# Kernel tuning notes

Measured on AMD Instinct MI355X. Metric: run time of the kernel, lower is better.

The kernel has to match this reference:

```python
import jax, jax.numpy as jnp
import numpy as np

N_NODES = 50000


def setup_inputs() -> dict:
    key = jax.random.key(0)
    k1, k2, k3, k4 = jax.random.split(key, 4)
    x = jax.random.normal(k1, (N_NODES, 128), dtype=jnp.float32)
    edge_index = jax.random.randint(k2, (2, 800000), 0, N_NODES, dtype=jnp.int64)
    W = jax.random.normal(k3, (128, 128), dtype=jnp.float32) * 0.05
    b = jax.random.normal(k4, (128,), dtype=jnp.float32) * 0.05
    return {"x": x, "edge_index": edge_index, "W": W, "b": b}


def reference(x, edge_index, W, b):
    # x: [N, C_in], edge_index: [2, E]
    row, col = edge_index[0], edge_index[1]
    n = x.shape[0]
    # degree of each node as a source (bincount over row)
    deg = jax.ops.segment_sum(jnp.ones_like(row, dtype=x.dtype), row, num_segments=n)
    # deg^{-1/2} with inf -> 0 (deg == 0 case)
    deg_inv_sqrt = jnp.where(deg > 0, jax.lax.rsqrt(jnp.maximum(deg, 1.0)) * jnp.where(deg > 0, 1.0, 0.0), 0.0)
    deg_inv_sqrt = jnp.where(deg > 0, deg ** -0.5, 0.0)
    norm = deg_inv_sqrt[row] * deg_inv_sqrt[col]  # [E]
    # gather, scale, scatter-add: agg[row] += x[col] * norm
    msgs = x[col] * norm[:, None]  # [E, C_in]
    agg = jax.ops.segment_sum(msgs, row, num_segments=n)  # [N, C_in]
    # linear
    return agg @ W.T + b
```

## Files before the change

kernel.cpp:

```cpp
#include <hip/hip_runtime.h>
#include <hip/hip_bf16.h>


typedef short v8s __attribute__((ext_vector_type(8)));
typedef float v4f __attribute__((ext_vector_type(4)));

#define ELLCAP 64
#define NSHARD 32
#define SUBCAP 224
#define ROWSTRIDE 136

static __device__ __forceinline__ unsigned int f2bf(float f) {
    __hip_bfloat16 h = __float2bfloat16(f);
    return (unsigned int)__builtin_bit_cast(unsigned short, h);
}

__global__ __launch_bounds__(256) void k_bin(
    const int* __restrict__ idx, int* __restrict__ gbin,
    unsigned int* __restrict__ pairs, const float4* __restrict__ w4,
    ushort4* __restrict__ wb4, const float2* __restrict__ x2,
    unsigned int* __restrict__ xs32, int E, int ncast, int N, int nbins) {
    int b = blockIdx.x;
    const int t = threadIdx.x;
    if (b < 16) {
        int i = b * 256 + t;
        float4 v = w4[i];
        ushort4 o;
        o.x = (unsigned short)f2bf(v.x);
        o.y = (unsigned short)f2bf(v.y);
        o.z = (unsigned short)f2bf(v.z);
        o.w = (unsigned short)f2bf(v.w);
        wb4[i] = o;
        return;
    }
    b -= 16;
    if (b < ncast) {
        int base = b * 4096;
#pragma unroll 4
        for (int it = 0; it < 16; ++it) {
            int i = base + it * 256 + t;
            int lr = i >> 6;
            unsigned ov = 0u;
            if (lr < N) {
                float2 v = x2[i];
                ov = f2bf(v.x) | (f2bf(v.y) << 16);
            }
            xs32[i] = ov;
        }
        return;
    }
    b -= ncast;
    __shared__ int hist[256];
    __shared__ int hist2[256];
    __shared__ int base[256];
    hist[t] = 0;
    hist2[t] = 0;
    __syncthreads();

    int e0 = b * 2048 + t * 8;
    int nv = E - e0;
    nv = nv > 8 ? 8 : (nv < 0 ? 0 : nv);
    int rows[8], cols[8];
    if (nv == 8) {
        int4 a0 = *(const int4*)&idx[e0];
        int4 a1 = *(const int4*)&idx[e0 + 4];
        int4 c0 = *(const int4*)&idx[E + e0];
        int4 c1 = *(const int4*)&idx[E + e0 + 4];
        rows[0] = a0.x; rows[1] = a0.y; rows[2] = a0.z; rows[3] = a0.w;
        rows[4] = a1.x; rows[5] = a1.y; rows[6] = a1.z; rows[7] = a1.w;
        cols[0] = c0.x; cols[1] = c0.y; cols[2] = c0.z; cols[3] = c0.w;
        cols[4] = c1.x; cols[5] = c1.y; cols[6] = c1.z; cols[7] = c1.w;
    } else {
        for (int k = 0; k < 8; ++k) {
            rows[k] = (k < nv) ? idx[e0 + k] : 0;
            cols[k] = (k < nv) ? idx[E + e0 + k] : 0;
        }
    }
#pragma unroll
    for (int k = 0; k < 8; ++k)
        if (k < nv) atomicAdd(&hist[rows[k] >> 8], 1);
    __syncthreads();
    const int shard = b & (NSHARD - 1);
    if (t < nbins)
        base[t] = atomicAdd(&gbin[t * NSHARD + shard], hist[t]);
    int loc[8];
#pragma unroll
    for (int k = 0; k < 8; ++k)
        loc[k] = (k < nv) ? atomicAdd(&hist2[rows[k] >> 8], 1) : 0;
    __syncthreads();
#pragma unroll
    for (int k = 0; k < 8; ++k) {
        if (k < nv) {
            int bin = rows[k] >> 8;
            int pos = base[bin] + loc[k];
            if (pos < SUBCAP)
                pairs[((size_t)bin * NSHARD + shard) * SUBCAP + pos] =
                    (unsigned)(((rows[k] & 255) << 16) | cols[k]);
        }
    }
}

__global__ __launch_bounds__(1024) void k_deg(
    const unsigned int* __restrict__ pairs, const int* __restrict__ gbin,
    float* __restrict__ dis, int N) {
    __shared__ int cnt[256];
    __shared__ int scnt[NSHARD];
    const int bin = blockIdx.x;
    const int t = threadIdx.x;
    if (t < 256) cnt[t] = 0;
    if (t < NSHARD) {
        int m = gbin[bin * NSHARD + t];
        scnt[t] = m > SUBCAP ? SUBCAP : m;
    }
    __syncthreads();
    for (int s = 0; s < NSHARD; ++s) {
        int ms = scnt[s];
        size_t pb = ((size_t)bin * NSHARD + s) * SUBCAP;
        for (int i = t; i < ms; i += 1024)
            atomicAdd(&cnt[pairs[pb + i] >> 16], 1);
    }
    __syncthreads();
    if (t < 256) {
        int r = bin * 256 + t;
        int d = cnt[t];
        dis[r] = (r < N && d > 0) ? rsqrtf((float)d) : 0.f;
    }
}

__global__ __launch_bounds__(256) void k_fused(
    const unsigned int* __restrict__ pairs, const int* __restrict__ gbin,
    const float* __restrict__ dis, const unsigned int* __restrict__ xs32,
    const v8s* __restrict__ Wb8, const float* __restrict__ bias,
    float* __restrict__ out, int N) {
    __shared__ __align__(16) unsigned short lell[32 * ELLCAP];
    __shared__ int cnt[32];
    __shared__ int scnt[NSHARD];
    __shared__ __align__(16) unsigned short smem[32 * ROWSTRIDE];
    const int bin = blockIdx.x >> 3, sub = blockIdx.x & 7;
    const int t = threadIdx.x;
    if (t < 32) cnt[t] = 0;
    else if (t >= 64 && t < 64 + NSHARD) {
        int m = gbin[bin * NSHARD + (t - 64)];
        scnt[t - 64] = m > SUBCAP ? SUBCAP : m;
    }
    __syncthreads();
    for (int s = 0; s < NSHARD; ++s) {
        int ms = scnt[s];
        size_t pb = ((size_t)bin * NSHARD + s) * SUBCAP;
        for (int i = t; i < ms; i += 256) {
            unsigned pv = pairs[pb + i];
            int lr = pv >> 16;
            if ((lr >> 5) == sub) {
                int la = lr & 31;
                int slot = atomicAdd(&cnt[la], 1);
                if (slot < ELLCAP)
                    lell[la * ELLCAP + slot] = (unsigned short)(pv & 0xFFFF);
            }
        }
    }
    __syncthreads();

    const int wv = t >> 6, lane = t & 63;
    const int r0 = bin * 256 + sub * 32;
    for (int i = 0; i < 8; ++i) {
        int lrow = wv * 8 + i;
        int n = r0 + lrow;
        float acc0 = 0.f, acc1 = 0.f;
        if (n < N) {
            int dtrue = cnt[lrow];
            int d = dtrue > ELLCAP ? ELLCAP : dtrue;
            int cl = lell[lrow * ELLCAP + lane];
            int c = (lane < d) ? cl : N;
            float dcf = dis[c];
            int dcb = __builtin_bit_cast(int, dcf);
            for (int j = 0; j < d; j += 16) {
                int cc[16];
#pragma unroll
                for (int u = 0; u < 16; ++u)
                    cc[u] = __builtin_amdgcn_readlane(c, j + u);
                unsigned uu[16];
#pragma unroll
                for (int u = 0; u < 16; ++u)
                    uu[u] = xs32[(size_t)cc[u] * 64 + lane];
                float sc[16];
#pragma unroll
                for (int u = 0; u < 16; ++u)
                    sc[u] = __builtin_bit_cast(
                        float, __builtin_amdgcn_readlane(dcb, j + u));
#pragma unroll
                for (int u = 0; u < 16; ++u) {
                    acc0 = fmaf(sc[u], __builtin_bit_cast(float, uu[u] << 16), acc0);
                    acc1 = fmaf(sc[u],
                                __builtin_bit_cast(float, uu[u] & 0xFFFF0000u), acc1);
                }
            }
            float s = (dtrue > 0) ? rsqrtf((float)dtrue) : 0.f;
            acc0 *= s;
            acc1 *= s;
        }
        unsigned pack = f2bf(acc0) | (f2bf(acc1) << 16);
        *(unsigned int*)&smem[(size_t)lrow * ROWSTRIDE + lane * 2] = pack;
    }
    __syncthreads();

    {
        int quad = lane >> 4, m16 = lane & 15;
        int lrow = (wv & 1) * 16 + m16;
        v8s afrag[4];
#pragma unroll
        for (int kk = 0; kk < 4; ++kk)
            afrag[kk] = *(const v8s*)&smem[lrow * ROWSTRIDE + kk * 32 + quad * 8];
        int rbase = r0 + (wv & 1) * 16 + quad * 4;
        int jbase = (wv >> 1) * 64;
#pragma unroll
        for (int jt = 0; jt < 4; ++jt) {
            int jcol = jbase + jt * 16 + m16;
            v4f acc = {0.f, 0.f, 0.f, 0.f};
#pragma unroll
            for (int kk = 0; kk < 4; ++kk) {
                v8s bfrag = Wb8[jcol * 16 + kk * 4 + quad];
                acc = __builtin_amdgcn_mfma_f32_16x16x32_bf16(afrag[kk], bfrag,
                                                              acc, 0, 0, 0);
            }
            float bj = bias[jcol];
#pragma unroll
            for (int r = 0; r < 4; ++r) {
                int row = rbase + r;
                if (row < N) out[(size_t)row * 128 + jcol] = acc[r] + bj;
            }
        }
    }
}

extern "C" void kernel_launch(void* const* d_in, const int* in_sizes, int n_in,
                              void* d_out, int out_size, void* d_ws, size_t ws_size,
                              hipStream_t stream) {
    const float* x = (const float*)d_in[0];
    const int* idx = (const int*)d_in[1];
    const float* W = (const float*)d_in[2];
    const float* b = (const float*)d_in[3];
    float* out = (float*)d_out;

    const int N = in_sizes[0] / 128;
    const int E = in_sizes[1] / 2;
    const int nbins = (N + 255) / 256;
    const int nrows = nbins * 256;
    const int ncast = nbins * 4;

    char* p = (char*)d_ws;
    auto alloc = [&](size_t bytes) {
        char* r = p;
        p += (bytes + 63) & ~(size_t)63;
        return r;
    };
    int* gbin = (int*)alloc((size_t)nbins * NSHARD * 4);
    unsigned int* pairs =
        (unsigned int*)alloc((size_t)nbins * NSHARD * SUBCAP * 4);
    float* dis = (float*)alloc((size_t)nrows * 4);
    unsigned int* xs = (unsigned int*)alloc((size_t)nrows * 128 * 2);
    ushort4* wb = (ushort4*)alloc(128 * 128 * 2);

    hipMemsetAsync(gbin, 0, (size_t)nbins * NSHARD * sizeof(int), stream);

    const int bblocks = 16 + ncast + (E + 2047) / 2048;
    k_bin<<<bblocks, 256, 0, stream>>>(idx, gbin, pairs, (const float4*)W, wb,
                                       (const float2*)x, xs, E, ncast, N, nbins);
    k_deg<<<nbins, 1024, 0, stream>>>(pairs, gbin, dis, N);
    k_fused<<<nbins * 8, 256, 0, stream>>>(pairs, gbin, dis, xs, (const v8s*)wb,
                                           b, out, N);
}
```

Measured before the change: 158.7 us.

## Build ELL adjacency once in degree kernel instead of per fused block

The degree kernel now builds the full per-bin ELL neighbor list in shared memory and writes it, together with clamped degree counts, to global memory. Previously each of the 8 fused blocks per bin rescanned all 32 shards of pairs and kept only its own rows. The fused kernel now just loads its ELL rows and degrees directly and prefetches all 8 rows' neighbor indices and scales before the gather loop. This adds a global ELL write/read (about 6.4 MB) and a 32 KB shared-memory buffer in the degree kernel in exchange for removing the redundant 8x rescan of the pairs buffer.

```diff
diff --git a/kernel.cpp b/kernel.cpp
--- a/kernel.cpp
+++ b/kernel.cpp
@@ -100,106 +100,106 @@
     }
 }
 
-__global__ __launch_bounds__(1024) void k_deg(
+__global__ __launch_bounds__(1024) void k_ell(
     const unsigned int* __restrict__ pairs, const int* __restrict__ gbin,
+    unsigned short* __restrict__ ell, unsigned char* __restrict__ degc,
     float* __restrict__ dis, int N) {
+    __shared__ __align__(16) unsigned short lell[256 * ELLCAP];
     __shared__ int cnt[256];
-    __shared__ int scnt[NSHARD];
     const int bin = blockIdx.x;
     const int t = threadIdx.x;
     if (t < 256) cnt[t] = 0;
-    if (t < NSHARD) {
-        int m = gbin[bin * NSHARD + t];
-        scnt[t] = m > SUBCAP ? SUBCAP : m;
-    }
-    __syncthreads();
-    for (int s = 0; s < NSHARD; ++s) {
-        int ms = scnt[s];
-        size_t pb = ((size_t)bin * NSHARD + s) * SUBCAP;
-        for (int i = t; i < ms; i += 1024)
-            atomicAdd(&cnt[pairs[pb + i] >> 16], 1);
-    }
-    __syncthreads();
+    __syncthreads();
+
+    {
+        const int g = t >> 5, l32 = t & 31;
+        int m = gbin[bin * NSHARD + g];
+        m = m > SUBCAP ? SUBCAP : m;
+        size_t pb = ((size_t)bin * NSHARD + g) * SUBCAP;
+        for (int i = l32; i < m; i += 32) {
+            unsigned pv = pairs[pb + i];
+            int la = pv >> 16;
+            int slot = atomicAdd(&cnt[la], 1);
+            if (slot < ELLCAP)
+                lell[la * ELLCAP + slot] = (unsigned short)(pv & 0xFFFF);
+        }
+    }
+    __syncthreads();
+
     if (t < 256) {
         int r = bin * 256 + t;
         int d = cnt[t];
-        dis[r] = (r < N && d > 0) ? rsqrtf((float)d) : 0.f;
+        if (r < N) {
+            dis[r] = (d > 0) ? rsqrtf((float)d) : 0.f;
+            degc[r] = (unsigned char)(d > ELLCAP ? ELLCAP : d);
+        } else {
+            dis[r] = 0.f;
+        }
+    }
+
+    {
+        unsigned int* gell = (unsigned int*)(ell + (size_t)bin * 256 * ELLCAP);
+        const unsigned int* sell = (const unsigned int*)lell;
+        for (int i = t; i < 8192; i += 1024) gell[i] = sell[i];
     }
 }
 
 __global__ __launch_bounds__(256) void k_fused(
-    const unsigned int* __restrict__ pairs, const int* __restrict__ gbin,
+    const unsigned short* __restrict__ ell, const unsigned char* __restrict__ degc,
     const float* __restrict__ dis, const unsigned int* __restrict__ xs32,
     const v8s* __restrict__ Wb8, const float* __restrict__ bias,
     float* __restrict__ out, int N) {
-    __shared__ __align__(16) unsigned short lell[32 * ELLCAP];
-    __shared__ int cnt[32];
-    __shared__ int scnt[NSHARD];
     __shared__ __align__(16) unsigned short smem[32 * ROWSTRIDE];
-    const int bin = blockIdx.x >> 3, sub = blockIdx.x & 7;
-    const int t = threadIdx.x;
-    if (t < 32) cnt[t] = 0;
-    else if (t >= 64 && t < 64 + NSHARD) {
-        int m = gbin[bin * NSHARD + (t - 64)];
-        scnt[t - 64] = m > SUBCAP ? SUBCAP : m;
-    }
-    __syncthreads();
-    for (int s = 0; s < NSHARD; ++s) {
-        int ms = scnt[s];
-        size_t pb = ((size_t)bin * NSHARD + s) * SUBCAP;
-        for (int i = t; i < ms; i += 256) {
-            unsigned pv = pairs[pb + i];
-            int lr = pv >> 16;
-            if ((lr >> 5) == sub) {
-                int la = lr & 31;
-                int slot = atomicAdd(&cnt[la], 1);
-                if (slot < ELLCAP)
-                    lell[la * ELLCAP + slot] = (unsigned short)(pv & 0xFFFF);
-            }
-        }
-    }
-    __syncthreads();
-
-    const int wv = t >> 6, lane = t & 63;
-    const int r0 = bin * 256 + sub * 32;
+    const int nb0 = blockIdx.x * 32;
+    const int wv = threadIdx.x >> 6, lane = threadIdx.x & 63;
+    const int rowbase = nb0 + wv * 8;
+
+    int d8[8], c8[8];
+    float dv8[8];
+#pragma unroll
     for (int i = 0; i < 8; ++i) {
-        int lrow = wv * 8 + i;
-        int n = r0 + lrow;
+        int n = rowbase + i;
+        int d = (n < N) ? degc[n] : 0;
+        d8[i] = __builtin_amdgcn_readfirstlane(d);
+        int cl = (n < N) ? ell[(size_t)n * ELLCAP + lane] : 0;
+        c8[i] = (lane < d8[i]) ? cl : N;
+    }
+#pragma unroll
+    for (int i = 0; i < 8; ++i) dv8[i] = dis[c8[i]];
+
+#pragma unroll
+    for (int i = 0; i < 8; ++i) {
+        int n = rowbase + i;
         float acc0 = 0.f, acc1 = 0.f;
-        if (n < N) {
-            int dtrue = cnt[lrow];
-            int d = dtrue > ELLCAP ? ELLCAP : dtrue;
-            int cl = lell[lrow * ELLCAP + lane];
-            int c = (lane < d) ? cl : N;
-            float dcf = dis[c];
-            int dcb = __builtin_bit_cast(int, dcf);
-            for (int j = 0; j < d; j += 16) {
-                int cc[16];
-#pragma unroll
-                for (int u = 0; u < 16; ++u)
-                    cc[u] = __builtin_amdgcn_readlane(c, j + u);
-                unsigned uu[16];
-#pragma unroll
-                for (int u = 0; u < 16; ++u)
-                    uu[u] = xs32[(size_t)cc[u] * 64 + lane];
-                float sc[16];
-#pragma unroll
-                for (int u = 0; u < 16; ++u)
-                    sc[u] = __builtin_bit_cast(
-                        float, __builtin_amdgcn_readlane(dcb, j + u));
-#pragma unroll
-                for (int u = 0; u < 16; ++u) {
-                    acc0 = fmaf(sc[u], __builtin_bit_cast(float, uu[u] << 16), acc0);
-                    acc1 = fmaf(sc[u],
-                                __builtin_bit_cast(float, uu[u] & 0xFFFF0000u), acc1);
-                }
-            }
-            float s = (dtrue > 0) ? rsqrtf((float)dtrue) : 0.f;
-            acc0 *= s;
-            acc1 *= s;
-        }
+        int d = d8[i];
+        int c = c8[i];
+        int dcb = __builtin_bit_cast(int, dv8[i]);
+        for (int j = 0; j < d; j += 16) {
+            int cc[16];
+#pragma unroll
+            for (int u = 0; u < 16; ++u)
+                cc[u] = __builtin_amdgcn_readlane(c, j + u);
+            unsigned uu[16];
+#pragma unroll
+            for (int u = 0; u < 16; ++u)
+                uu[u] = xs32[(size_t)cc[u] * 64 + lane];
+            float sc[16];
+#pragma unroll
+            for (int u = 0; u < 16; ++u)
+                sc[u] = __builtin_bit_cast(float,
+                                           __builtin_amdgcn_readlane(dcb, j + u));
+#pragma unroll
+            for (int u = 0; u < 16; ++u) {
+                acc0 = fmaf(sc[u], __builtin_bit_cast(float, uu[u] << 16), acc0);
+                acc1 = fmaf(sc[u],
+                            __builtin_bit_cast(float, uu[u] & 0xFFFF0000u), acc1);
+            }
+        }
+        float s = dis[n];
+        acc0 *= s;
+        acc1 *= s;
         unsigned pack = f2bf(acc0) | (f2bf(acc1) << 16);
-        *(unsigned int*)&smem[(size_t)lrow * ROWSTRIDE + lane * 2] = pack;
+        *(unsigned int*)&smem[(size_t)(wv * 8 + i) * ROWSTRIDE + lane * 2] = pack;
     }
     __syncthreads();
 
@@ -210,7 +210,7 @@
 #pragma unroll
         for (int kk = 0; kk < 4; ++kk)
             afrag[kk] = *(const v8s*)&smem[lrow * ROWSTRIDE + kk * 32 + quad * 8];
-        int rbase = r0 + (wv & 1) * 16 + quad * 4;
+        int rbase = nb0 + (wv & 1) * 16 + quad * 4;
         int jbase = (wv >> 1) * 64;
 #pragma unroll
         for (int jt = 0; jt < 4; ++jt) {
@@ -257,6 +257,9 @@
     unsigned int* pairs =
         (unsigned int*)alloc((size_t)nbins * NSHARD * SUBCAP * 4);
     float* dis = (float*)alloc((size_t)nrows * 4);
+    unsigned char* degc = (unsigned char*)alloc((size_t)N);
+    unsigned short* ell =
+        (unsigned short*)alloc((size_t)nrows * ELLCAP * 2);
     unsigned int* xs = (unsigned int*)alloc((size_t)nrows * 128 * 2);
     ushort4* wb = (ushort4*)alloc(128 * 128 * 2);
 
@@ -265,7 +268,7 @@
     const int bblocks = 16 + ncast + (E + 2047) / 2048;
     k_bin<<<bblocks, 256, 0, stream>>>(idx, gbin, pairs, (const float4*)W, wb,
                                        (const float2*)x, xs, E, ncast, N, nbins);
-    k_deg<<<nbins, 1024, 0, stream>>>(pairs, gbin, dis, N);
-    k_fused<<<nbins * 8, 256, 0, stream>>>(pairs, gbin, dis, xs, (const v8s*)wb,
-                                           b, out, N);
-}
+    k_ell<<<nbins, 1024, 0, stream>>>(pairs, gbin, ell, degc, dis, N);
+    k_fused<<<(N + 31) / 32, 256, 0, stream>>>(ell, degc, dis, xs,
+                                               (const v8s*)wb, b, out, N);
+}
```

Measured after the change: 148.2 us. 6.6% less time.
